# Performance work log

Hardware: AMD Instinct MI355X
Metric: run time of the kernel (lower is better)

The kernel has to match this reference:

```python
import jax, jax.numpy as jnp
import numpy as np
from jax import lax

# Balloon-Windkessel BOLD hemodynamic model, explicit Euler, 1000 steps.
# getEulerBOLD(mtt, kappa=1.0, gamma=1.0, stim_on=True, n_steps=1000)
# States: s (vasodilatory signal), f (inflow), v (blood volume), q (deoxyhemoglobin).
# BOLD readout: y = V0*(k1*(1-q) + k2*(1 - q/v) + k3*(1 - v))

N_STEPS = 1000
DT = 0.01           # Euler step (s)
ALPHA = 0.32        # Grubb's exponent
RHO = 0.34          # resting oxygen extraction fraction
V0 = 0.02           # resting blood volume fraction
K1 = 7.0 * RHO
K2 = 2.0
K3 = 2.0 * RHO - 0.2
KAPPA = 1.0         # signal decay (2nd arg in source)
GAMMA = 1.0         # flow-dependent elimination (3rd arg in source)


def _euler_bold(mtt):
    u = jnp.ones((N_STEPS,), dtype=mtt.dtype)  # stimulus on (True flag)
    inv_alpha = 1.0 / ALPHA

    def step(carry, u_t):
        s, f, v, q = carry
        v_pow = v ** inv_alpha                       # outflow f_out(v) = v^(1/alpha)
        E = 1.0 - (1.0 - RHO) ** (1.0 / f)           # oxygen extraction E(f)
        ds = u_t - KAPPA * s - GAMMA * (f - 1.0)
        df = s
        dv = (f - v_pow) / mtt
        dq = (f * E / RHO - v_pow * q / v) / mtt
        s = s + DT * ds
        f = f + DT * df
        v = v + DT * dv
        q = q + DT * dq
        y = V0 * (K1 * (1.0 - q) + K2 * (1.0 - q / v) + K3 * (1.0 - v))
        return (s, f, v, q), y

    one = jnp.asarray(1.0, dtype=mtt.dtype)
    zero = jnp.asarray(0.0, dtype=mtt.dtype)
    init = (zero, one, one, one)
    _, ys = lax.scan(step, init, u)
    return ys  # [N_STEPS]


def setup_inputs() -> dict:
    mtt = jnp.asarray(1.0, dtype=jnp.float32)  # nn.Parameter(torch.tensor(1.0))
    return {"mtt": mtt}


def reference(mtt) -> jnp.ndarray:
    return _euler_bold(mtt)
```

## Files before the change

### kernel.cpp

```cpp
#include <hip/hip_runtime.h>
#include <math.h>


namespace {
constexpr int   kSteps  = 1000;
constexpr int   kChunks = 250;
constexpr int   kSweeps = 6;
constexpr float kDt     = 0.01f;
constexpr float kInvRho = 1.0f / 0.34f;
constexpr float kV0 = 0.02f, kK1 = 2.38f, kK2 = 2.0f, kK3 = 0.48f;
constexpr float kLog2R    = -0.0071769251f;
constexpr float kThetaRev =  0.0013852133f;
constexpr float kCB       = -0.57735026919f;
constexpr float kL2OneMR  = -0.5994620704f;
constexpr float kPwm1     = 2.125f;
}

__global__ __launch_bounds__(256)
void bold_kernel(const void* __restrict__ mtt_raw, float* __restrict__ out) {
    __shared__ __align__(16) float Xb[kSteps];
    __shared__ float2 SC[4];
    const int tid  = threadIdx.x;
    const int lane = tid & 63, wid = tid >> 6;

    unsigned bits = *(const unsigned*)mtt_raw;
    float mtt = ((bits & 0xFFFFu) == 0u) ? __uint_as_float(bits)
                                         : __uint_as_float(bits << 16);
    const float c1   = kDt / mtt;
    const float c31  = 3.125f * c1;
    const float c21  = kPwm1 * c1;

    float Fc[4], Bq[4];
    if (tid < kChunks) {
        #pragma unroll
        for (int k = 0; k < 4; ++k) {
            float tf = (float)(4 * tid + k);
            float rt = __builtin_amdgcn_exp2f(tf * kLog2R);
            float ar = tf * kThetaRev;
            float sn = __builtin_amdgcn_sinf(ar);
            float cs = __builtin_amdgcn_cosf(ar);
            float ft = fmaf(rt, fmaf(kCB, sn, -cs), 2.0f);
            float E1 = __builtin_amdgcn_exp2f(kL2OneMR * __builtin_amdgcn_rcpf(ft));
            Fc[k] = c1 * ft;
            Bq[k] = (c1 * kInvRho) * ft * (1.0f - E1);
        }
        ((float4*)Xb)[tid] = make_float4(1.f, 1.f, 1.f, 1.f);
    }
    __syncthreads();

    float A[4], B[4];

    for (int sweep = 0; sweep < kSweeps; ++sweep) {
        float Pc = 1.0f, Qc = 0.0f;
        if (tid < kChunks) {
            float4 X   = ((float4*)Xb)[tid];
            float pred = (tid == 0) ? 1.0f : Xb[4 * tid - 1];
            float vb[4] = {pred, X.x, X.y, X.z};
            #pragma unroll
            for (int k = 0; k < 4; ++k) {
                float vt = vb[k];
                float w  = __builtin_amdgcn_exp2f(
                               kPwm1 * __builtin_amdgcn_logf(vt));
                float p3 = w * vt;
                float At = fmaf(-c31, w, 1.0f);
                float Bt = fmaf(c21, p3, Fc[k]);
                A[k] = At; B[k] = Bt;
                Qc = fmaf(At, Qc, Bt);
                Pc = At * Pc;
            }
        }
        float xP = Pc, xQ = Qc;
        #pragma unroll
        for (int off = 1; off < 64; off <<= 1) {
            float yP = __shfl_up(xP, off, 64);
            float yQ = __shfl_up(xQ, off, 64);
            if (lane >= off) { xQ = fmaf(xP, yQ, xQ); xP *= yP; }
        }
        if (lane == 63) SC[wid] = make_float2(xP, xQ);
        __syncthreads();
        float eP = __shfl_up(xP, 1, 64);
        float eQ = __shfl_up(xQ, 1, 64);
        if (lane == 0) { eP = 1.0f; eQ = 0.0f; }
        float wP = 1.0f, wQ = 0.0f;
        for (int w2 = 0; w2 < wid; ++w2) {
            float2 a = SC[w2];
            wQ = fmaf(a.x, wQ, a.y);
            wP = a.x * wP;
        }
        float EP = eP * wP;
        float EQ = fmaf(eP, wQ, eQ);
        if (tid < kChunks) {
            float x = EP + EQ;
            float4 Xn;
            x = fmaf(A[0], x, B[0]); Xn.x = x;
            x = fmaf(A[1], x, B[1]); Xn.y = x;
            x = fmaf(A[2], x, B[2]); Xn.z = x;
            x = fmaf(A[3], x, B[3]); Xn.w = x;
            ((float4*)Xb)[tid] = Xn;
        }
        __syncthreads();
    }

    float Vx[4];
    {
        float Pc = 1.0f, Qc = 0.0f;
        if (tid < kChunks) {
            float4 X   = ((float4*)Xb)[tid];
            float pred = (tid == 0) ? 1.0f : Xb[4 * tid - 1];
            float vb[4] = {pred, X.x, X.y, X.z};
            Vx[0] = X.x; Vx[1] = X.y; Vx[2] = X.z; Vx[3] = X.w;
            #pragma unroll
            for (int k = 0; k < 4; ++k) {
                float w  = __builtin_amdgcn_exp2f(
                               kPwm1 * __builtin_amdgcn_logf(vb[k]));
                float At = fmaf(-c1, w, 1.0f);
                A[k] = At;
                Qc = fmaf(At, Qc, Bq[k]);
                Pc = At * Pc;
            }
        }
        float xP = Pc, xQ = Qc;
        #pragma unroll
        for (int off = 1; off < 64; off <<= 1) {
            float yP = __shfl_up(xP, off, 64);
            float yQ = __shfl_up(xQ, off, 64);
            if (lane >= off) { xQ = fmaf(xP, yQ, xQ); xP *= yP; }
        }
        if (lane == 63) SC[wid] = make_float2(xP, xQ);
        __syncthreads();
        float eP = __shfl_up(xP, 1, 64);
        float eQ = __shfl_up(xQ, 1, 64);
        if (lane == 0) { eP = 1.0f; eQ = 0.0f; }
        float wP = 1.0f, wQ = 0.0f;
        for (int w2 = 0; w2 < wid; ++w2) {
            float2 a = SC[w2];
            wQ = fmaf(a.x, wQ, a.y);
            wP = a.x * wP;
        }
        float EP = eP * wP;
        float EQ = fmaf(eP, wQ, eQ);
        if (tid < kChunks) {
            float q = EP + EQ;
            float yv[4];
            #pragma unroll
            for (int k = 0; k < 4; ++k) {
                q = fmaf(A[k], q, Bq[k]);
                float vn = Vx[k];
                yv[k] = kV0 * (kK1 * (1.0f - q)
                             + kK2 * fmaf(-q, __builtin_amdgcn_rcpf(vn), 1.0f)
                             + kK3 * (1.0f - vn));
            }
            ((float4*)out)[tid] = make_float4(yv[0], yv[1], yv[2], yv[3]);
        }
    }
}

extern "C" void kernel_launch(void* const* d_in, const int* in_sizes, int n_in,
                              void* d_out, int out_size, void* d_ws, size_t ws_size,
                              hipStream_t stream) {
    bold_kernel<<<dim3(1), dim3(256), 0, stream>>>(d_in[0], (float*)d_out);
}
```

Baseline: 56.14 us.

## Cut fixed-point sweeps, use DPP wave scans, fuse final v and q scans

Lowers the number of Picard-style sweeps over v from six to a closed-form first sweep plus four, with the last sweep fused with the q scan. Keeps the v state in registers instead of shared memory, passing chunk boundaries through shuffles and a small per-wave shared array. Replaces the shfl_up-based wave scan with DPP row-shift/broadcast steps and unrolls the cross-wave combine. Fewer sweeps may change the accuracy of the v fixed point, so convergence tolerance is at risk.

```diff
diff --git a/kernel.cpp b/kernel.cpp
--- a/kernel.cpp
+++ b/kernel.cpp
@@ -3,9 +3,7 @@
 
 
 namespace {
-constexpr int   kSteps  = 1000;
 constexpr int   kChunks = 250;
-constexpr int   kSweeps = 6;
 constexpr float kDt     = 0.01f;
 constexpr float kInvRho = 1.0f / 0.34f;
 constexpr float kV0 = 0.02f, kK1 = 2.38f, kK2 = 2.0f, kK3 = 0.48f;
@@ -16,21 +14,49 @@
 constexpr float kPwm1     = 2.125f;
 }
 
+template<int Ctrl, int RowMask>
+__device__ __forceinline__ float dppf(float x, float ident) {
+    return __int_as_float(__builtin_amdgcn_update_dpp(
+        __float_as_int(ident), __float_as_int(x), Ctrl, RowMask, 0xF, false));
+}
+
+__device__ __forceinline__ void wave_scan2(float& xP, float& xQ) {
+    #define ST(C, M) { float yP = dppf<C, M>(xP, 1.0f);            \
+                       float yQ = dppf<C, M>(xQ, 0.0f);            \
+                       xQ = fmaf(xP, yQ, xQ); xP *= yP; }
+    ST(0x111, 0xF) ST(0x112, 0xF) ST(0x114, 0xF) ST(0x118, 0xF)
+    ST(0x142, 0xA) ST(0x143, 0xC)
+    #undef ST
+}
+__device__ __forceinline__ void wave_scan4(float& xP, float& xQ,
+                                           float& uP, float& uQ) {
+    #define ST(C, M) { float yP = dppf<C, M>(xP, 1.0f);            \
+                       float yQ = dppf<C, M>(xQ, 0.0f);            \
+                       float zP = dppf<C, M>(uP, 1.0f);            \
+                       float zQ = dppf<C, M>(uQ, 0.0f);            \
+                       xQ = fmaf(xP, yQ, xQ); xP *= yP;            \
+                       uQ = fmaf(uP, zQ, uQ); uP *= zP; }
+    ST(0x111, 0xF) ST(0x112, 0xF) ST(0x114, 0xF) ST(0x118, 0xF)
+    ST(0x142, 0xA) ST(0x143, 0xC)
+    #undef ST
+}
+
 __global__ __launch_bounds__(256)
 void bold_kernel(const void* __restrict__ mtt_raw, float* __restrict__ out) {
-    __shared__ __align__(16) float Xb[kSteps];
-    __shared__ float2 SC[4];
+    __shared__ float2 SCv[4];
+    __shared__ float2 SCq[4];
+    __shared__ float  SCX[4];
     const int tid  = threadIdx.x;
     const int lane = tid & 63, wid = tid >> 6;
 
     unsigned bits = *(const unsigned*)mtt_raw;
     float mtt = ((bits & 0xFFFFu) == 0u) ? __uint_as_float(bits)
                                          : __uint_as_float(bits << 16);
-    const float c1   = kDt / mtt;
-    const float c31  = 3.125f * c1;
-    const float c21  = kPwm1 * c1;
-
-    float Fc[4], Bq[4];
+    const float c1  = kDt / mtt;
+    const float c31 = 3.125f * c1;
+    const float c21 = kPwm1 * c1;
+
+    float Fc[4] = {0, 0, 0, 0}, Bq[4] = {0, 0, 0, 0};
     if (tid < kChunks) {
         #pragma unroll
         for (int k = 0; k < 4; ++k) {
@@ -44,111 +70,127 @@
             Fc[k] = c1 * ft;
             Bq[k] = (c1 * kInvRho) * ft * (1.0f - E1);
         }
-        ((float4*)Xb)[tid] = make_float4(1.f, 1.f, 1.f, 1.f);
-    }
-    __syncthreads();
-
-    float A[4], B[4];
-
-    for (int sweep = 0; sweep < kSweeps; ++sweep) {
+    }
+
+    float4 X = make_float4(1.f, 1.f, 1.f, 1.f);
+    float A[4] = {1, 1, 1, 1}, B[4] = {0, 0, 0, 0};
+
+    {
         float Pc = 1.0f, Qc = 0.0f;
-        if (tid < kChunks) {
-            float4 X   = ((float4*)Xb)[tid];
-            float pred = (tid == 0) ? 1.0f : Xb[4 * tid - 1];
-            float vb[4] = {pred, X.x, X.y, X.z};
-            #pragma unroll
-            for (int k = 0; k < 4; ++k) {
-                float vt = vb[k];
+        const float A0 = 1.0f - c31;
+        if (tid < kChunks) {
+            #pragma unroll
+            for (int k = 0; k < 4; ++k) {
+                A[k] = A0; B[k] = Fc[k] + c21;
+                Qc = fmaf(A0, Qc, B[k]); Pc *= A0;
+            }
+        }
+        float xP = Pc, xQ = Qc;
+        wave_scan2(xP, xQ);
+        if (lane == 63) SCv[wid] = make_float2(xP, xQ);
+        __syncthreads();
+        float eP = __shfl_up(xP, 1, 64), eQ = __shfl_up(xQ, 1, 64);
+        if (lane == 0) { eP = 1.f; eQ = 0.f; }
+        float2 a0 = SCv[0], a1 = SCv[1], a2 = SCv[2];
+        float wP = 1.f, wQ = 0.f;
+        if (wid >= 1) { wP = a0.x; wQ = a0.y; }
+        if (wid >= 2) { wQ = fmaf(a1.x, wQ, a1.y); wP *= a1.x; }
+        if (wid >= 3) { wQ = fmaf(a2.x, wQ, a2.y); wP *= a2.x; }
+        float x = fmaf(eP, wQ, eQ) + eP * wP;
+        x = fmaf(A[0], x, B[0]); X.x = x;
+        x = fmaf(A[1], x, B[1]); X.y = x;
+        x = fmaf(A[2], x, B[2]); X.z = x;
+        x = fmaf(A[3], x, B[3]); X.w = x;
+        if (lane == 63) SCX[wid] = X.w;
+        __syncthreads();
+    }
+
+    for (int sw = 0; sw < 3; ++sw) {
+        float predw = __shfl_up(X.w, 1, 64);
+        float oldw  = (wid == 0) ? 1.0f : SCX[wid - 1];
+        if (lane == 0) predw = oldw;
+        float Pc = 1.0f, Qc = 0.0f;
+        if (tid < kChunks) {
+            float vb[4] = {predw, X.x, X.y, X.z};
+            #pragma unroll
+            for (int k = 0; k < 4; ++k) {
                 float w  = __builtin_amdgcn_exp2f(
-                               kPwm1 * __builtin_amdgcn_logf(vt));
-                float p3 = w * vt;
+                               kPwm1 * __builtin_amdgcn_logf(vb[k]));
+                float p3 = w * vb[k];
                 float At = fmaf(-c31, w, 1.0f);
                 float Bt = fmaf(c21, p3, Fc[k]);
                 A[k] = At; B[k] = Bt;
-                Qc = fmaf(At, Qc, Bt);
-                Pc = At * Pc;
+                Qc = fmaf(At, Qc, Bt); Pc = At * Pc;
             }
         }
         float xP = Pc, xQ = Qc;
-        #pragma unroll
-        for (int off = 1; off < 64; off <<= 1) {
-            float yP = __shfl_up(xP, off, 64);
-            float yQ = __shfl_up(xQ, off, 64);
-            if (lane >= off) { xQ = fmaf(xP, yQ, xQ); xP *= yP; }
-        }
-        if (lane == 63) SC[wid] = make_float2(xP, xQ);
-        __syncthreads();
-        float eP = __shfl_up(xP, 1, 64);
-        float eQ = __shfl_up(xQ, 1, 64);
-        if (lane == 0) { eP = 1.0f; eQ = 0.0f; }
-        float wP = 1.0f, wQ = 0.0f;
-        for (int w2 = 0; w2 < wid; ++w2) {
-            float2 a = SC[w2];
-            wQ = fmaf(a.x, wQ, a.y);
-            wP = a.x * wP;
-        }
-        float EP = eP * wP;
-        float EQ = fmaf(eP, wQ, eQ);
-        if (tid < kChunks) {
-            float x = EP + EQ;
-            float4 Xn;
-            x = fmaf(A[0], x, B[0]); Xn.x = x;
-            x = fmaf(A[1], x, B[1]); Xn.y = x;
-            x = fmaf(A[2], x, B[2]); Xn.z = x;
-            x = fmaf(A[3], x, B[3]); Xn.w = x;
-            ((float4*)Xb)[tid] = Xn;
-        }
-        __syncthreads();
-    }
-
-    float Vx[4];
+        wave_scan2(xP, xQ);
+        if (lane == 63) SCv[wid] = make_float2(xP, xQ);
+        __syncthreads();
+        float eP = __shfl_up(xP, 1, 64), eQ = __shfl_up(xQ, 1, 64);
+        if (lane == 0) { eP = 1.f; eQ = 0.f; }
+        float2 a0 = SCv[0], a1 = SCv[1], a2 = SCv[2];
+        float wP = 1.f, wQ = 0.f;
+        if (wid >= 1) { wP = a0.x; wQ = a0.y; }
+        if (wid >= 2) { wQ = fmaf(a1.x, wQ, a1.y); wP *= a1.x; }
+        if (wid >= 3) { wQ = fmaf(a2.x, wQ, a2.y); wP *= a2.x; }
+        float x = fmaf(eP, wQ, eQ) + eP * wP;
+        x = fmaf(A[0], x, B[0]); X.x = x;
+        x = fmaf(A[1], x, B[1]); X.y = x;
+        x = fmaf(A[2], x, B[2]); X.z = x;
+        x = fmaf(A[3], x, B[3]); X.w = x;
+        if (lane == 63) SCX[wid] = X.w;
+        __syncthreads();
+    }
+
     {
-        float Pc = 1.0f, Qc = 0.0f;
-        if (tid < kChunks) {
-            float4 X   = ((float4*)Xb)[tid];
-            float pred = (tid == 0) ? 1.0f : Xb[4 * tid - 1];
-            float vb[4] = {pred, X.x, X.y, X.z};
-            Vx[0] = X.x; Vx[1] = X.y; Vx[2] = X.z; Vx[3] = X.w;
-            #pragma unroll
-            for (int k = 0; k < 4; ++k) {
-                float w  = __builtin_amdgcn_exp2f(
-                               kPwm1 * __builtin_amdgcn_logf(vb[k]));
-                float At = fmaf(-c1, w, 1.0f);
-                A[k] = At;
-                Qc = fmaf(At, Qc, Bq[k]);
-                Pc = At * Pc;
-            }
-        }
-        float xP = Pc, xQ = Qc;
-        #pragma unroll
-        for (int off = 1; off < 64; off <<= 1) {
-            float yP = __shfl_up(xP, off, 64);
-            float yQ = __shfl_up(xQ, off, 64);
-            if (lane >= off) { xQ = fmaf(xP, yQ, xQ); xP *= yP; }
-        }
-        if (lane == 63) SC[wid] = make_float2(xP, xQ);
-        __syncthreads();
-        float eP = __shfl_up(xP, 1, 64);
-        float eQ = __shfl_up(xQ, 1, 64);
-        if (lane == 0) { eP = 1.0f; eQ = 0.0f; }
-        float wP = 1.0f, wQ = 0.0f;
-        for (int w2 = 0; w2 < wid; ++w2) {
-            float2 a = SC[w2];
-            wQ = fmaf(a.x, wQ, a.y);
-            wP = a.x * wP;
-        }
-        float EP = eP * wP;
-        float EQ = fmaf(eP, wQ, eQ);
-        if (tid < kChunks) {
-            float q = EP + EQ;
+        float predw = __shfl_up(X.w, 1, 64);
+        float oldw  = (wid == 0) ? 1.0f : SCX[wid - 1];
+        if (lane == 0) predw = oldw;
+        float Pv = 1.f, Qv = 0.f, Pq = 1.f, Qq = 0.f;
+        float Aq[4] = {1, 1, 1, 1};
+        if (tid < kChunks) {
+            float vb[4] = {predw, X.x, X.y, X.z};
+            #pragma unroll
+            for (int k = 0; k < 4; ++k) {
+                float w   = __builtin_amdgcn_exp2f(
+                                kPwm1 * __builtin_amdgcn_logf(vb[k]));
+                float p3  = w * vb[k];
+                float At  = fmaf(-c31, w, 1.0f);
+                float Bt  = fmaf(c21, p3, Fc[k]);
+                float Aqt = fmaf(-c1, w, 1.0f);
+                A[k] = At; B[k] = Bt; Aq[k] = Aqt;
+                Qv = fmaf(At, Qv, Bt);     Pv = At * Pv;
+                Qq = fmaf(Aqt, Qq, Bq[k]); Pq = Aqt * Pq;
+            }
+        }
+        float xP = Pv, xQ = Qv, uP = Pq, uQ = Qq;
+        wave_scan4(xP, xQ, uP, uQ);
+        if (lane == 63) { SCv[wid] = make_float2(xP, xQ);
+                          SCq[wid] = make_float2(uP, uQ); }
+        __syncthreads();
+        float eP = __shfl_up(xP, 1, 64), eQ = __shfl_up(xQ, 1, 64);
+        float fP = __shfl_up(uP, 1, 64), fQ = __shfl_up(uQ, 1, 64);
+        if (lane == 0) { eP = 1.f; eQ = 0.f; fP = 1.f; fQ = 0.f; }
+        float2 a0 = SCv[0], a1 = SCv[1], a2 = SCv[2];
+        float2 b0 = SCq[0], b1 = SCq[1], b2 = SCq[2];
+        float wP = 1.f, wQ = 0.f, vP = 1.f, vQ = 0.f;
+        if (wid >= 1) { wP = a0.x; wQ = a0.y; vP = b0.x; vQ = b0.y; }
+        if (wid >= 2) { wQ = fmaf(a1.x, wQ, a1.y); wP *= a1.x;
+                        vQ = fmaf(b1.x, vQ, b1.y); vP *= b1.x; }
+        if (wid >= 3) { wQ = fmaf(a2.x, wQ, a2.y); wP *= a2.x;
+                        vQ = fmaf(b2.x, vQ, b2.y); vP *= b2.x; }
+        if (tid < kChunks) {
+            float x = fmaf(eP, wQ, eQ) + eP * wP;
+            float q = fmaf(fP, vQ, fQ) + fP * vP;
             float yv[4];
             #pragma unroll
             for (int k = 0; k < 4; ++k) {
-                q = fmaf(A[k], q, Bq[k]);
-                float vn = Vx[k];
+                x = fmaf(A[k],  x, B[k]);
+                q = fmaf(Aq[k], q, Bq[k]);
                 yv[k] = kV0 * (kK1 * (1.0f - q)
-                             + kK2 * fmaf(-q, __builtin_amdgcn_rcpf(vn), 1.0f)
-                             + kK3 * (1.0f - vn));
+                             + kK2 * fmaf(-q, __builtin_amdgcn_rcpf(x), 1.0f)
+                             + kK3 * (1.0f - x));
             }
             ((float4*)out)[tid] = make_float4(yv[0], yv[1], yv[2], yv[3]);
         }
```

Result: faster. 53.50 us (-4.7%).
